# Kernel optimization log

Hardware: AMD Instinct MI355X
Metric: run time of the kernel (lower is better)

## Reference

```python
import jax, jax.numpy as jnp
import numpy as np

jax.config.update("jax_enable_x64", True)  # FixedPointMul math is done in float64, as in torch

B, S, H = 8, 4096, 768


def setup_inputs():
    key = jax.random.key(0)
    k = jax.random.split(key, 6)
    s_act = jnp.array([4.0 / 127.0], dtype=jnp.float32)  # per-tensor 8-bit activation scale

    def qact(kk):  # produce int8-quantized-looking activations
        x = jax.random.normal(kk, (B, S, H), jnp.float32)
        return s_act * jnp.clip(jnp.round(x / s_act), -128, 127)

    return {
        "hidden_states": qact(k[0]),
        "hidden_states_scaling_factor": s_act,
        "input_tensor": qact(k[1]),
        "input_tensor_scaling_factor": s_act,
        "dense_weight": 0.02 * jax.random.normal(k[2], (H, H), jnp.float32),
        "dense_bias": 0.01 * jax.random.normal(k[3], (H,), jnp.float32),
        "ln_weight": 1.0 + 0.05 * jax.random.normal(k[4], (H,), jnp.float32),
        "ln_bias": 0.05 * jax.random.normal(k[5], (H,), jnp.float32),
    }


def _sym_scale(k, smin, smax):
    n = 2 ** (k - 1) - 1
    return jnp.clip(jnp.maximum(jnp.abs(smin), jnp.abs(smax)), 1e-8, None) / n


def _sym_quant(x, k, scale):
    n = 2 ** (k - 1) - 1
    return jnp.clip(jnp.round(x / scale), -n, n - 1)


def _batch_frexp(x):
    # returns (round(mantissa * 2^31), 31 - exponent) as in ibert batch_frexp
    m, e = jnp.frexp(x)
    return jnp.floor(m * (2.0 ** 31) + 0.5), 31.0 - e


def _fixedpoint_mul(x, pre_scale, bit, z_scale, identity=None, id_scale=None):
    n = 2 ** (bit - 1) - 1
    ps = jnp.reshape(pre_scale, (1, 1, -1)).astype(jnp.float64)
    z = z_scale.astype(jnp.float64)
    z_int = jnp.round(x.astype(jnp.float64) / ps)
    m, e = _batch_frexp(ps / z)
    out = jnp.round(z_int * m / (2.0 ** e))
    if identity is not None:
        isf = jnp.reshape(id_scale, (1, 1, -1)).astype(jnp.float64)
        wx = jnp.round(identity.astype(jnp.float64) / isf)
        m1, e1 = _batch_frexp(isf / z)
        out = out + jnp.round(wx * m1 / (2.0 ** e1))
    return jnp.clip(out, -n - 1, n).astype(jnp.float32)


def _quant_act(x, bit, pre_scale, identity=None, id_scale=None):
    x_act = x if identity is None else x + identity
    s = _sym_scale(bit, x_act.min(), x_act.max())  # per-tensor scale (dynamic range)
    q = _fixedpoint_mul(x, pre_scale, bit, s, identity, id_scale)
    return q * s, s


def reference(hidden_states, hidden_states_scaling_factor, input_tensor, input_tensor_scaling_factor, dense_weight, dense_bias, ln_weight, ln_bias):
    # ---- QuantLinear: per-channel int8 weights, int32 bias ----
    w_min = dense_weight.min(axis=1)
    w_max = dense_weight.max(axis=1)
    fc_scale = _sym_scale(8, w_min, w_max)                      # [H_out]
    w_int = _sym_quant(dense_weight, 8, fc_scale[:, None])      # [H_out, H_in]
    bias_scale = fc_scale * hidden_states_scaling_factor        # [H_out]
    b_int = _sym_quant(dense_bias, 32, bias_scale)
    x_int = hidden_states / hidden_states_scaling_factor
    hs = (jnp.einsum("bsh,oh->bso", x_int, w_int) + b_int) * bias_scale
    # dropout: eval mode -> identity
    # ---- QuantAct(22-bit) with quantized residual add ----
    hs, ln_in_scale = _quant_act(hs, 22, bias_scale, input_tensor, input_tensor_scaling_factor)
    # ---- IntLayerNorm (integer-only LayerNorm) ----
    x_int = hs / ln_in_scale
    mean_int = jnp.round(jnp.mean(x_int, axis=2, keepdims=True))
    y_int = x_int - mean_int
    var0 = jnp.sum(y_int ** 2, axis=2, keepdims=True)
    shift = jnp.ceil(jnp.log2(jnp.sqrt(jnp.maximum(var0, 1.0) / 2.0 ** 32)))  # set_shift (max_bit=32)
    shift = jnp.maximum(0.0, shift.max())
    y_sh = jnp.floor(y_int / 2.0 ** shift)
    var_int = jnp.sum(y_sh ** 2, axis=2, keepdims=True)
    std_int = jnp.floor(jnp.sqrt(var_int)) * 2.0 ** shift
    factor = jnp.floor(2.0 ** 31 / std_int)
    y_int = jnp.floor(y_int * factor / 2.0)
    sf = jnp.sqrt(jnp.float32(H)) / 2.0 ** 30
    bias_int = jnp.floor((ln_bias / ln_weight) / sf)
    y_int = y_int + bias_int
    sf_out = sf * ln_weight                                     # [H]
    hs = y_int * sf_out
    # ---- QuantAct(8-bit) output requantization ----
    hs, out_scale = _quant_act(hs, 8, sf_out)
    return hs, out_scale
```

## Files before the change

### kernel.cpp

```cpp
#include <hip/hip_runtime.h>

typedef int   v4i   __attribute__((ext_vector_type(4)));
typedef unsigned long u64x2 __attribute__((ext_vector_type(2)));

#define HDIM 768
#define NTOK 32768

static constexpr size_t WX_OFF   = 0;
static constexpr size_t WINT_OFF = 25165824;
static constexpr size_t FACT_OFF = WINT_OFF + 589824;
static constexpr size_t RS1_OFF  = WINT_OFF + 1179648;
static constexpr size_t RS2_OFF  = RS1_OFF + 6144;
static constexpr size_t BS_OFF   = RS2_OFF + 6144;
static constexpr size_t BINT_OFF = BS_OFF + 3072;
static constexpr size_t LNBI_OFF = BINT_OFF + 3072;
static constexpr size_t SFO_OFF  = LNBI_OFF + 3072;
static constexpr size_t SC_OFF   = SFO_OFF + 3072;
static constexpr size_t RSM1_OFF = SC_OFF + 64;

__device__ __forceinline__ unsigned fenc(float f) {
    unsigned u = __float_as_uint(f);
    return (u >> 31) ? ~u : (u | 0x80000000u);
}
__device__ __forceinline__ float fdec(unsigned e) {
    unsigned u = (e >> 31) ? (e & 0x7fffffffu) : ~e;
    return __uint_as_float(u);
}

#define GLDS16(g, l) __builtin_amdgcn_global_load_lds( \
    (const __attribute__((address_space(1))) unsigned int*)(g), \
    (__attribute__((address_space(3))) unsigned int*)(l), 16, 0, 0)

__device__ __forceinline__ int swz4(int r) { return (r & 3) ^ ((r >> 2) & 3); }

__global__ __launch_bounds__(256) void k0_prep(const float* __restrict__ W,
                                               const float* __restrict__ bias,
                                               const float* __restrict__ ln_w,
                                               const float* __restrict__ ln_b,
                                               const float* __restrict__ phsf,
                                               char* __restrict__ ws) {
    int o = blockIdx.x, tid = threadIdx.x;
    __shared__ float red[256];
    __shared__ float fc_sh;
    float m = 0.f;
    for (int j = tid; j < HDIM; j += 256) m = fmaxf(m, fabsf(W[(size_t)o * HDIM + j]));
    red[tid] = m;
    __syncthreads();
    for (int s = 128; s; s >>= 1) { if (tid < s) red[tid] = fmaxf(red[tid], red[tid + s]); __syncthreads(); }
    if (tid == 0) {
        float fc = fmaxf(red[0], 1e-8f) / 127.0f;
        float hsf = *phsf;
        float bs = fc * hsf;
        fc_sh = fc;
        ((float*)(ws + BS_OFF))[o] = bs;
        ((int*)(ws + BINT_OFF))[o] = (int)rintf(bias[o] / bs);
        float sf = sqrtf(768.0f) / 1073741824.0f;
        float lw = ln_w[o], lb = ln_b[o];
        ((int*)(ws + LNBI_OFF))[o] = (int)floorf((lb / lw) / sf);
        ((float*)(ws + SFO_OFF))[o] = sf * lw;
    }
    __syncthreads();
    float fc = fc_sh;
    char* w8 = (char*)(ws + WINT_OFF);
    for (int j = tid; j < HDIM; j += 256) {
        float q = rintf(W[(size_t)o * HDIM + j] / fc);
        q = fminf(fmaxf(q, -127.f), 126.f);
        w8[(size_t)o * HDIM + j] = (char)q;
    }
    if (blockIdx.x == 0 && tid < 8) {
        unsigned* sc = (unsigned*)(ws + SC_OFF);
        unsigned v = 0u;
        if (tid == 0 || tid == 2) v = 0xFFFFFFFFu;
        sc[tid] = v;
    }
}

__global__ __launch_bounds__(256) void kp_a8(const float* __restrict__ hs,
                                             const float* __restrict__ phsf,
                                             char* __restrict__ ws) {
    int idx = blockIdx.x * 256 + threadIdx.x;
    float inv = 1.0f / *phsf;
    const float4* in4 = (const float4*)hs + (size_t)idx * 4;
    unsigned ow[4];
    #pragma unroll
    for (int j = 0; j < 4; ++j) {
        float4 v = in4[j];
        int q0 = (int)rintf(v.x * inv), q1 = (int)rintf(v.y * inv);
        int q2 = (int)rintf(v.z * inv), q3 = (int)rintf(v.w * inv);
        ow[j] = (unsigned)(q0 & 255) | ((unsigned)(q1 & 255) << 8) |
                ((unsigned)(q2 & 255) << 16) | ((unsigned)(q3 & 255) << 24);
    }
    ((uint4*)(ws + WX_OFF))[idx] = make_uint4(ow[0], ow[1], ow[2], ow[3]);
}

#define BM 128
#define BN 192
#define BK 64
#define NKT (HDIM / BK)
__global__ __launch_bounds__(256) void k1_gemm(const float* __restrict__ inp,
                                               char* __restrict__ ws,
                                               int* __restrict__ accOut) {
    __shared__ alignas(16) char As[2][BM * BK];
    __shared__ alignas(16) char Bs[2][BN * BK];
    __shared__ float rmn[4], rmx[4];
    int tid = threadIdx.x, lane = tid & 63, wave = tid >> 6;
    int wrow = lane & 15, g = lane >> 4;
    int bid = blockIdx.x;
    int xcd = bid & 7, slot = bid >> 3;
    int mtile = xcd * 32 + (slot >> 2);
    int ntile = slot & 3;
    int t0 = mtile * BM, o0 = ntile * BN;
    const char* a8 = (const char*)(ws + WX_OFF);
    const char* w8 = (const char*)(ws + WINT_OFF);

    const char* asrc[2]; const char* bsrc[3];
    int aldso[2], bldso[3];
    #pragma unroll
    for (int i = 0; i < 2; ++i) {
        int c = i * 256 + tid, r = c >> 2, s = c & 3;
        asrc[i] = a8 + (size_t)(t0 + r) * HDIM + (s ^ swz4(r)) * 16;
        aldso[i] = (i * 256 + wave * 64) * 16;
    }
    #pragma unroll
    for (int i = 0; i < 3; ++i) {
        int c = i * 256 + tid, r = c >> 2, s = c & 3;
        bsrc[i] = w8 + (size_t)(o0 + r) * HDIM + (s ^ swz4(r)) * 16;
        bldso[i] = (i * 256 + wave * 64) * 16;
    }

    int wm = wave & 1, wn = wave >> 1;
    int aofs[4], bofs[6];
    #pragma unroll
    for (int mi = 0; mi < 4; ++mi) { int r = wm * 64 + mi * 16 + wrow; aofs[mi] = r * BK + ((g ^ swz4(r)) * 16); }
    #pragma unroll
    for (int nf = 0; nf < 6; ++nf) { int r = wn * 96 + nf * 16 + wrow; bofs[nf] = r * BK + ((g ^ swz4(r)) * 16); }

    #pragma unroll
    for (int i = 0; i < 2; ++i) GLDS16(asrc[i], &As[0][aldso[i]]);
    #pragma unroll
    for (int i = 0; i < 3; ++i) GLDS16(bsrc[i], &Bs[0][bldso[i]]);
    #pragma unroll
    for (int i = 0; i < 2; ++i) GLDS16(asrc[i] + BK, &As[1][aldso[i]]);
    #pragma unroll
    for (int i = 0; i < 3; ++i) GLDS16(bsrc[i] + BK, &Bs[1][bldso[i]]);
    asm volatile("s_waitcnt vmcnt(5)" ::: "memory");
    __builtin_amdgcn_s_barrier();

    v4i acc[4][6] = {};
    for (int kt = 0; kt < NKT; ++kt) {
        int cur = kt & 1;
        u64x2 af[4], bf[6];
        #pragma unroll
        for (int mi = 0; mi < 4; ++mi) af[mi] = *(const u64x2*)&As[cur][aofs[mi]];
        #pragma unroll
        for (int nf = 0; nf < 6; ++nf) bf[nf] = *(const u64x2*)&Bs[cur][bofs[nf]];
        asm volatile("s_waitcnt lgkmcnt(0)" ::: "memory");
        __builtin_amdgcn_s_barrier();
        if (kt + 2 < NKT) {
            #pragma unroll
            for (int i = 0; i < 2; ++i) GLDS16(asrc[i] + (kt + 2) * BK, &As[cur][aldso[i]]);
            #pragma unroll
            for (int i = 0; i < 3; ++i) GLDS16(bsrc[i] + (kt + 2) * BK, &Bs[cur][bldso[i]]);
        }
        __builtin_amdgcn_s_setprio(1);
        #pragma unroll
        for (int mi = 0; mi < 4; ++mi)
            #pragma unroll
            for (int nf = 0; nf < 6; ++nf) {
                acc[mi][nf] = __builtin_amdgcn_mfma_i32_16x16x32_i8((long)af[mi][0], (long)bf[nf][0], acc[mi][nf], 0, 0, 0);
                acc[mi][nf] = __builtin_amdgcn_mfma_i32_16x16x32_i8((long)af[mi][1], (long)bf[nf][1], acc[mi][nf], 0, 0, 0);
            }
        __builtin_amdgcn_s_setprio(0);
        if (kt + 2 < NKT) {
            asm volatile("s_waitcnt vmcnt(5)" ::: "memory");
            __builtin_amdgcn_s_barrier();
        } else if (kt + 2 == NKT) {
            asm volatile("s_waitcnt vmcnt(0)" ::: "memory");
            __builtin_amdgcn_s_barrier();
        }
    }

    const float* bscale = (const float*)(ws + BS_OFF);
    const int* bint = (const int*)(ws + BINT_OFF);
    int oo[6]; float bsc[6]; int bi[6];
    #pragma unroll
    for (int nf = 0; nf < 6; ++nf) {
        oo[nf] = o0 + wn * 96 + nf * 16 + wrow;
        bsc[nf] = bscale[oo[nf]];
        bi[nf]  = bint[oo[nf]];
    }
    float lmn = 3.402823466e38f, lmx = -3.402823466e38f;
    #pragma unroll
    for (int mi = 0; mi < 4; ++mi)
        #pragma unroll
        for (int r = 0; r < 4; ++r) {
            int t = t0 + wm * 64 + mi * 16 + g * 4 + r;
            size_t rb = (size_t)t * HDIM;
            #pragma unroll
            for (int nf = 0; nf < 6; ++nf) {
                int a = acc[mi][nf][r] + bi[nf];
                size_t idx = rb + oo[nf];
                accOut[idx] = a;
                float xa = (float)a * bsc[nf] + inp[idx];
                lmn = fminf(lmn, xa);
                lmx = fmaxf(lmx, xa);
            }
        }
    #pragma unroll
    for (int off = 32; off; off >>= 1) {
        lmn = fminf(lmn, __shfl_down(lmn, off));
        lmx = fmaxf(lmx, __shfl_down(lmx, off));
    }
    if (lane == 0) { rmn[wave] = lmn; rmx[wave] = lmx; }
    __syncthreads();
    if (tid == 0) {
        float mn = fminf(fminf(rmn[0], rmn[1]), fminf(rmn[2], rmn[3]));
        float mx = fmaxf(fmaxf(rmx[0], rmx[1]), fmaxf(rmx[2], rmx[3]));
        volatile unsigned* sc = (volatile unsigned*)(ws + SC_OFF);
        unsigned emn = fenc(mn), emx = fenc(mx);
        if (emn < sc[0]) atomicMin((unsigned*)&sc[0], emn);
        if (emx > sc[1]) atomicMax((unsigned*)&sc[1], emx);
    }
}

__global__ __launch_bounds__(256) void k2_scale1(const float* __restrict__ pisf, char* __restrict__ ws) {
    __shared__ float s_sh;
    unsigned* sc = (unsigned*)(ws + SC_OFF);
    if (threadIdx.x == 0) {
        float mn = fdec(sc[0]), mx = fdec(sc[1]);
        float s = fmaxf(fmaxf(fabsf(mn), fabsf(mx)), 1e-8f) / 2097151.0f;
        ((float*)sc)[5] = s;
        s_sh = s;
        double r = (double)(*pisf) / (double)s;
        int ex; double mant = frexp(r, &ex);
        double m1 = floor(mant * 2147483648.0 + 0.5);
        ((double*)(ws + RSM1_OFF))[0] = m1 * exp2((double)(ex - 31));
    }
    __syncthreads();
    float s = s_sh;
    const float* bs = (const float*)(ws + BS_OFF);
    double* rs1 = (double*)(ws + RS1_OFF);
    for (int o = threadIdx.x; o < HDIM; o += 256) {
        double r = (double)bs[o] / (double)s;
        int ex; double mant = frexp(r, &ex);
        double m = floor(mant * 2147483648.0 + 0.5);
        rs1[o] = m * exp2((double)(ex - 31));
    }
}

__global__ __launch_bounds__(256) void k3_rows(char* __restrict__ ws, int* __restrict__ buf,
                                               const float* __restrict__ inp,
                                               const float* __restrict__ pisf) {
    int tid = threadIdx.x, lane = tid & 63, wave = tid >> 6;
    int wid = blockIdx.x * 4 + wave;
    const double* rs1 = (const double*)(ws + RS1_OFF);
    double rsm1 = *(const double*)(ws + RSM1_OFF);
    float inv_isf = 1.0f / *pisf;
    double t_rs1[12];
    #pragma unroll
    for (int c = 0; c < 3; ++c) {
        int o0 = (lane + 64 * c) * 4;
        #pragma unroll
        for (int j = 0; j < 4; ++j) t_rs1[c * 4 + j] = rs1[o0 + j];
    }
    int localShift = 0;
    int4 aP[3]; float4 xP[3];
    {
        size_t b0 = (size_t)(wid * 4) * HDIM;
        #pragma unroll
        for (int c = 0; c < 3; ++c) {
            aP[c] = ((const int4*)(buf + b0))[lane + 64 * c];
            xP[c] = ((const float4*)(inp + b0))[lane + 64 * c];
        }
    }
    for (int rr = 0; rr < 4; ++rr) {
        int4 aN[3]; float4 xN[3];
        if (rr < 3) {
            size_t nb = (size_t)(wid * 4 + rr + 1) * HDIM;
            #pragma unroll
            for (int c = 0; c < 3; ++c) {
                aN[c] = ((const int4*)(buf + nb))[lane + 64 * c];
                xN[c] = ((const float4*)(inp + nb))[lane + 64 * c];
            }
        }
        size_t base = (size_t)(wid * 4 + rr) * HDIM;
        int q[12];
        int sum = 0;
        #pragma unroll
        for (int c = 0; c < 3; ++c) {
            int av[4] = {aP[c].x, aP[c].y, aP[c].z, aP[c].w};
            float xv[4] = {xP[c].x, xP[c].y, xP[c].z, xP[c].w};
            #pragma unroll
            for (int j = 0; j < 4; ++j) {
                double q1 = rint((double)av[j] * t_rs1[c * 4 + j]);
                int wxj = (int)rintf(xv[j] * inv_isf);
                double qq = q1 + rint((double)wxj * rsm1);
                qq = fmin(fmax(qq, -2097152.0), 2097151.0);
                q[c * 4 + j] = (int)qq;
                sum += q[c * 4 + j];
            }
        }
        #pragma unroll
        for (int off = 32; off; off >>= 1) sum += __shfl_xor(sum, off);
        int mean = (int)rint((double)sum / 768.0);
        long long var0 = 0;
        #pragma unroll
        for (int k = 0; k < 12; ++k) { q[k] -= mean; var0 += (long long)q[k] * (long long)q[k]; }
        #pragma unroll
        for (int off = 32; off; off >>= 1) var0 += __shfl_xor(var0, off);
        #pragma unroll
        for (int c = 0; c < 3; ++c) {
            int4 y = {q[c * 4 + 0], q[c * 4 + 1], q[c * 4 + 2], q[c * 4 + 3]};
            ((int4*)(buf + base))[lane + 64 * c] = y;
        }
        if (lane == 0) {
            double v = (double)(var0 < 1 ? 1LL : var0);
            int sr = (int)ceil(0.5 * log2(v) - 16.0);
            localShift = max(localShift, sr);
        }
        #pragma unroll
        for (int c = 0; c < 3; ++c) { aP[c] = aN[c]; xP[c] = xN[c]; }
    }
    if (lane == 0 && localShift > 0) {
        int* sp = (int*)(ws + SC_OFF) + 4;
        if (localShift > *(volatile int*)sp) atomicMax(sp, localShift);
    }
}

__global__ __launch_bounds__(256) void k4_rows(char* __restrict__ ws, const int* __restrict__ buf) {
    int tid = threadIdx.x, lane = tid & 63, wave = tid >> 6;
    int wid = blockIdx.x * 4 + wave;
    int shift = *(((const int*)(ws + SC_OFF)) + 4);
    const int* lnbi = (const int*)(ws + LNBI_OFF);
    const float* sfo = (const float*)(ws + SFO_OFF);
    __shared__ float rmn[4], rmx[4];
    int t_lnbi[12]; float t_sfo[12];
    #pragma unroll
    for (int c = 0; c < 3; ++c) {
        int o0 = (lane + 64 * c) * 4;
        #pragma unroll
        for (int j = 0; j < 4; ++j) { t_lnbi[c * 4 + j] = lnbi[o0 + j]; t_sfo[c * 4 + j] = sfo[o0 + j]; }
    }
    unsigned* fact = (unsigned*)(ws + FACT_OFF);
    float lmn = 3.402823466e38f, lmx = -3.402823466e38f;
    int4 yP[3];
    {
        size_t b0 = (size_t)(wid * 4) * HDIM;
        #pragma unroll
        for (int c = 0; c < 3; ++c) yP[c] = ((const int4*)(buf + b0))[lane + 64 * c];
    }
    for (int rr = 0; rr < 4; ++rr) {
        int4 yN[3];
        if (rr < 3) {
            size_t nb = (size_t)(wid * 4 + rr + 1) * HDIM;
            #pragma unroll
            for (int c = 0; c < 3; ++c) yN[c] = ((const int4*)(buf + nb))[lane + 64 * c];
        }
        int yv[12];
        #pragma unroll
        for (int c = 0; c < 3; ++c) {
            yv[c * 4 + 0] = yP[c].x; yv[c * 4 + 1] = yP[c].y; yv[c * 4 + 2] = yP[c].z; yv[c * 4 + 3] = yP[c].w;
        }
        long long var = 0;
        #pragma unroll
        for (int k = 0; k < 12; ++k) { int ysh = yv[k] >> shift; var += (long long)ysh * (long long)ysh; }
        #pragma unroll
        for (int off = 32; off; off >>= 1) var += __shfl_xor(var, off);
        double std_int = floor(sqrt((double)var)) * (double)(1LL << shift);
        if (std_int < 1.0) std_int = 1.0;
        long long factor = (long long)floor(2147483648.0 / std_int);
        if (lane == 0) fact[wid * 4 + rr] = (unsigned)factor;
        #pragma unroll
        for (int k = 0; k < 12; ++k) {
            long long t = ((long long)yv[k] * factor) >> 1;
            int v2 = (int)t + t_lnbi[k];
            float h = (float)v2 * t_sfo[k];
            lmn = fminf(lmn, h);
            lmx = fmaxf(lmx, h);
        }
        #pragma unroll
        for (int c = 0; c < 3; ++c) yP[c] = yN[c];
    }
    #pragma unroll
    for (int off = 32; off; off >>= 1) {
        lmn = fminf(lmn, __shfl_xor(lmn, off));
        lmx = fmaxf(lmx, __shfl_xor(lmx, off));
    }
    if (lane == 0) { rmn[wave] = lmn; rmx[wave] = lmx; }
    __syncthreads();
    if (tid == 0) {
        float mn = fminf(fminf(rmn[0], rmn[1]), fminf(rmn[2], rmn[3]));
        float mx = fmaxf(fmaxf(rmx[0], rmx[1]), fmaxf(rmx[2], rmx[3]));
        volatile unsigned* sc = (volatile unsigned*)(ws + SC_OFF);
        unsigned emn = fenc(mn), emx = fenc(mx);
        if (emn < sc[2]) atomicMin((unsigned*)&sc[2], emn);
        if (emx > sc[3]) atomicMax((unsigned*)&sc[3], emx);
    }
}

__global__ __launch_bounds__(256) void k5_scale2(char* __restrict__ ws) {
    __shared__ float s_sh;
    unsigned* sc = (unsigned*)(ws + SC_OFF);
    if (threadIdx.x == 0) {
        float mn = fdec(sc[2]), mx = fdec(sc[3]);
        float s2 = fmaxf(fmaxf(fabsf(mn), fabsf(mx)), 1e-8f) / 127.0f;
        ((float*)sc)[6] = s2;
        s_sh = s2;
    }
    __syncthreads();
    float s2 = s_sh;
    const float* sfo = (const float*)(ws + SFO_OFF);
    double* rs2 = (double*)(ws + RS2_OFF);
    for (int o = threadIdx.x; o < HDIM; o += 256) {
        double r = (double)sfo[o] / (double)s2;
        int ex; double mant = frexp(r, &ex);
        double m = floor(mant * 2147483648.0 + 0.5);
        rs2[o] = m * exp2((double)(ex - 31));
    }
}

__global__ __launch_bounds__(256) void k6_out(char* __restrict__ ws, float* __restrict__ out) {
    int tid = threadIdx.x, lane = tid & 63, wave = tid >> 6;
    int wid = blockIdx.x * 4 + wave;
    const double* rs2 = (const double*)(ws + RS2_OFF);
    const int* lnbi = (const int*)(ws + LNBI_OFF);
    const unsigned* fact = (const unsigned*)(ws + FACT_OFF);
    float s2 = ((const float*)(ws + SC_OFF))[6];
    double t_rs2[12]; int t_lnbi[12];
    #pragma unroll
    for (int c = 0; c < 3; ++c) {
        int o0 = (lane + 64 * c) * 4;
        #pragma unroll
        for (int j = 0; j < 4; ++j) { t_rs2[c * 4 + j] = rs2[o0 + j]; t_lnbi[c * 4 + j] = lnbi[o0 + j]; }
    }
    int* buf = (int*)out;
    int4 yP[3];
    {
        size_t b0 = (size_t)(wid * 4) * HDIM;
        #pragma unroll
        for (int c = 0; c < 3; ++c) yP[c] = ((const int4*)(buf + b0))[lane + 64 * c];
    }
    for (int rr = 0; rr < 4; ++rr) {
        int4 yN[3];
        if (rr < 3) {
            size_t nb = (size_t)(wid * 4 + rr + 1) * HDIM;
            #pragma unroll
            for (int c = 0; c < 3; ++c) yN[c] = ((const int4*)(buf + nb))[lane + 64 * c];
        }
        size_t base = (size_t)(wid * 4 + rr) * HDIM;
        long long factor = (long long)fact[wid * 4 + rr];
        int yv[12];
        #pragma unroll
        for (int c = 0; c < 3; ++c) {
            yv[c * 4 + 0] = yP[c].x; yv[c * 4 + 1] = yP[c].y; yv[c * 4 + 2] = yP[c].z; yv[c * 4 + 3] = yP[c].w;
        }
        #pragma unroll
        for (int c = 0; c < 3; ++c) {
            float4 r;
            float* rp = &r.x;
            #pragma unroll
            for (int j = 0; j < 4; ++j) {
                int k = c * 4 + j;
                long long t = ((long long)yv[k] * factor) >> 1;
                int v2 = (int)t + t_lnbi[k];
                double q = rint((double)v2 * t_rs2[k]);
                q = fmin(fmax(q, -128.0), 127.0);
                rp[j] = (float)q * s2;
            }
            ((float4*)(out + base))[lane + 64 * c] = r;
        }
        #pragma unroll
        for (int c = 0; c < 3; ++c) yP[c] = yN[c];
    }
    if (wid == 0 && tid == 0) out[(size_t)NTOK * HDIM] = s2;
}

extern "C" void kernel_launch(void* const* d_in, const int* in_sizes, int n_in,
                              void* d_out, int out_size, void* d_ws, size_t ws_size,
                              hipStream_t stream) {
    const float* hs   = (const float*)d_in[0];
    const float* phsf = (const float*)d_in[1];
    const float* inp  = (const float*)d_in[2];
    const float* pisf = (const float*)d_in[3];
    const float* W    = (const float*)d_in[4];
    const float* bias = (const float*)d_in[5];
    const float* ln_w = (const float*)d_in[6];
    const float* ln_b = (const float*)d_in[7];
    char* ws = (char*)d_ws;
    float* out = (float*)d_out;
    int* buf = (int*)d_out;

    k0_prep<<<HDIM, 256, 0, stream>>>(W, bias, ln_w, ln_b, phsf, ws);
    kp_a8<<<NTOK * HDIM / 4096, 256, 0, stream>>>(hs, phsf, ws);
    k1_gemm<<<(NTOK / BM) * (HDIM / BN), 256, 0, stream>>>(inp, ws, buf);
    k2_scale1<<<1, 256, 0, stream>>>(pisf, ws);
    k3_rows<<<NTOK / 16, 256, 0, stream>>>(ws, buf, inp, pisf);
    k4_rows<<<NTOK / 16, 256, 0, stream>>>(ws, buf);
    k5_scale2<<<1, 256, 0, stream>>>(ws);
    k6_out<<<NTOK / 16, 256, 0, stream>>>(ws, out);
}
```

Measured before the change: 412.7 us.

## Quantize residual input to int8 once and stage GEMM epilogue through LDS

The activation prep kernel now also quantizes the residual input to int8 in workspace. The GEMM epilogue and the first row kernel then read 1 byte per element instead of a float. The GEMM epilogue writes accumulators into shared memory and re-reads them as row-contiguous int4 chunks, which gives coalesced global stores and loads. The int8 path is gated on workspace size, which adds an extra buffer and extra barriers in the epilogue.

```diff
diff --git a/kernel.cpp b/kernel.cpp
--- a/kernel.cpp
+++ b/kernel.cpp
@@ -17,6 +17,8 @@
 static constexpr size_t SFO_OFF  = LNBI_OFF + 3072;
 static constexpr size_t SC_OFF   = SFO_OFF + 3072;
 static constexpr size_t RSM1_OFF = SC_OFF + 64;
+static constexpr size_t INP8_OFF = RSM1_OFF + 64;
+static constexpr size_t WS_NEED8 = INP8_OFF + (size_t)NTOK * HDIM;
 
 __device__ __forceinline__ unsigned fenc(float f) {
     unsigned u = __float_as_uint(f);
@@ -75,34 +77,57 @@
     }
 }
 
+template<int U8>
 __global__ __launch_bounds__(256) void kp_a8(const float* __restrict__ hs,
+                                             const float* __restrict__ inp,
                                              const float* __restrict__ phsf,
+                                             const float* __restrict__ pisf,
                                              char* __restrict__ ws) {
     int idx = blockIdx.x * 256 + threadIdx.x;
-    float inv = 1.0f / *phsf;
-    const float4* in4 = (const float4*)hs + (size_t)idx * 4;
+    float invh = 1.0f / *phsf;
+    const float4* h4 = (const float4*)hs + (size_t)idx * 4;
     unsigned ow[4];
     #pragma unroll
     for (int j = 0; j < 4; ++j) {
-        float4 v = in4[j];
-        int q0 = (int)rintf(v.x * inv), q1 = (int)rintf(v.y * inv);
-        int q2 = (int)rintf(v.z * inv), q3 = (int)rintf(v.w * inv);
+        float4 v = h4[j];
+        int q0 = (int)rintf(v.x * invh), q1 = (int)rintf(v.y * invh);
+        int q2 = (int)rintf(v.z * invh), q3 = (int)rintf(v.w * invh);
         ow[j] = (unsigned)(q0 & 255) | ((unsigned)(q1 & 255) << 8) |
                 ((unsigned)(q2 & 255) << 16) | ((unsigned)(q3 & 255) << 24);
     }
     ((uint4*)(ws + WX_OFF))[idx] = make_uint4(ow[0], ow[1], ow[2], ow[3]);
+    if (U8) {
+        float invi = 1.0f / *pisf;
+        const float4* x4 = (const float4*)inp + (size_t)idx * 4;
+        unsigned oi[4];
+        #pragma unroll
+        for (int j = 0; j < 4; ++j) {
+            float4 v = x4[j];
+            int q0 = (int)rintf(v.x * invi), q1 = (int)rintf(v.y * invi);
+            int q2 = (int)rintf(v.z * invi), q3 = (int)rintf(v.w * invi);
+            oi[j] = (unsigned)(q0 & 255) | ((unsigned)(q1 & 255) << 8) |
+                    ((unsigned)(q2 & 255) << 16) | ((unsigned)(q3 & 255) << 24);
+        }
+        ((uint4*)(ws + INP8_OFF))[idx] = make_uint4(oi[0], oi[1], oi[2], oi[3]);
+    }
 }
 
 #define BM 128
 #define BN 192
 #define BK 64
 #define NKT (HDIM / BK)
+#define SROW 196
+template<int U8>
 __global__ __launch_bounds__(256) void k1_gemm(const float* __restrict__ inp,
+                                               const char* __restrict__ i8,
+                                               const float* __restrict__ pisf,
                                                char* __restrict__ ws,
                                                int* __restrict__ accOut) {
-    __shared__ alignas(16) char As[2][BM * BK];
-    __shared__ alignas(16) char Bs[2][BN * BK];
-    __shared__ float rmn[4], rmx[4];
+    __shared__ alignas(16) char smem[40992];
+    char* As0 = smem;
+    char* Bs0 = smem + 16384;
+    float* rmn = (float*)(smem + 40960);
+    float* rmx = rmn + 4;
     int tid = threadIdx.x, lane = tid & 63, wave = tid >> 6;
     int wrow = lane & 15, g = lane >> 4;
     int bid = blockIdx.x;
@@ -136,31 +161,33 @@
     for (int nf = 0; nf < 6; ++nf) { int r = wn * 96 + nf * 16 + wrow; bofs[nf] = r * BK + ((g ^ swz4(r)) * 16); }
 
     #pragma unroll
-    for (int i = 0; i < 2; ++i) GLDS16(asrc[i], &As[0][aldso[i]]);
-    #pragma unroll
-    for (int i = 0; i < 3; ++i) GLDS16(bsrc[i], &Bs[0][bldso[i]]);
-    #pragma unroll
-    for (int i = 0; i < 2; ++i) GLDS16(asrc[i] + BK, &As[1][aldso[i]]);
-    #pragma unroll
-    for (int i = 0; i < 3; ++i) GLDS16(bsrc[i] + BK, &Bs[1][bldso[i]]);
+    for (int i = 0; i < 2; ++i) GLDS16(asrc[i], As0 + aldso[i]);
+    #pragma unroll
+    for (int i = 0; i < 3; ++i) GLDS16(bsrc[i], Bs0 + bldso[i]);
+    #pragma unroll
+    for (int i = 0; i < 2; ++i) GLDS16(asrc[i] + BK, As0 + 8192 + aldso[i]);
+    #pragma unroll
+    for (int i = 0; i < 3; ++i) GLDS16(bsrc[i] + BK, Bs0 + 12288 + bldso[i]);
     asm volatile("s_waitcnt vmcnt(5)" ::: "memory");
     __builtin_amdgcn_s_barrier();
 
     v4i acc[4][6] = {};
     for (int kt = 0; kt < NKT; ++kt) {
         int cur = kt & 1;
+        const char* Ac = As0 + cur * 8192;
+        const char* Bc = Bs0 + cur * 12288;
         u64x2 af[4], bf[6];
         #pragma unroll
-        for (int mi = 0; mi < 4; ++mi) af[mi] = *(const u64x2*)&As[cur][aofs[mi]];
-        #pragma unroll
-        for (int nf = 0; nf < 6; ++nf) bf[nf] = *(const u64x2*)&Bs[cur][bofs[nf]];
+        for (int mi = 0; mi < 4; ++mi) af[mi] = *(const u64x2*)(Ac + aofs[mi]);
+        #pragma unroll
+        for (int nf = 0; nf < 6; ++nf) bf[nf] = *(const u64x2*)(Bc + bofs[nf]);
         asm volatile("s_waitcnt lgkmcnt(0)" ::: "memory");
         __builtin_amdgcn_s_barrier();
         if (kt + 2 < NKT) {
             #pragma unroll
-            for (int i = 0; i < 2; ++i) GLDS16(asrc[i] + (kt + 2) * BK, &As[cur][aldso[i]]);
-            #pragma unroll
-            for (int i = 0; i < 3; ++i) GLDS16(bsrc[i] + (kt + 2) * BK, &Bs[cur][bldso[i]]);
+            for (int i = 0; i < 2; ++i) GLDS16(asrc[i] + (kt + 2) * BK, As0 + cur * 8192 + aldso[i]);
+            #pragma unroll
+            for (int i = 0; i < 3; ++i) GLDS16(bsrc[i] + (kt + 2) * BK, Bs0 + cur * 12288 + bldso[i]);
         }
         __builtin_amdgcn_s_setprio(1);
         #pragma unroll
@@ -182,35 +209,54 @@
 
     const float* bscale = (const float*)(ws + BS_OFF);
     const int* bint = (const int*)(ws + BINT_OFF);
-    int oo[6]; float bsc[6]; int bi[6];
-    #pragma unroll
-    for (int nf = 0; nf < 6; ++nf) {
-        oo[nf] = o0 + wn * 96 + nf * 16 + wrow;
-        bsc[nf] = bscale[oo[nf]];
-        bi[nf]  = bint[oo[nf]];
-    }
+    float isf = U8 ? *pisf : 0.f;
+    int* sAcc = (int*)smem;
     float lmn = 3.402823466e38f, lmx = -3.402823466e38f;
     #pragma unroll
-    for (int mi = 0; mi < 4; ++mi)
-        #pragma unroll
-        for (int r = 0; r < 4; ++r) {
-            int t = t0 + wm * 64 + mi * 16 + g * 4 + r;
-            size_t rb = (size_t)t * HDIM;
-            #pragma unroll
-            for (int nf = 0; nf < 6; ++nf) {
-                int a = acc[mi][nf][r] + bi[nf];
-                size_t idx = rb + oo[nf];
-                accOut[idx] = a;
-                float xa = (float)a * bsc[nf] + inp[idx];
-                lmn = fminf(lmn, xa);
-                lmx = fmaxf(lmx, xa);
+    for (int mi = 0; mi < 4; ++mi) {
+        __syncthreads();
+        #pragma unroll
+        for (int nf = 0; nf < 6; ++nf)
+            #pragma unroll
+            for (int r = 0; r < 4; ++r)
+                sAcc[(wm * 16 + g * 4 + r) * SROW + wn * 96 + nf * 16 + wrow] = acc[mi][nf][r];
+        __syncthreads();
+        #pragma unroll
+        for (int k = 0; k < 6; ++k) {
+            int i4 = tid + k * 256;
+            int sr = i4 / 48, c4 = i4 - sr * 48;
+            int t = t0 + (sr >> 4) * 64 + mi * 16 + (sr & 15);
+            int col = o0 + c4 * 4;
+            int4 a4 = *(const int4*)&sAcc[sr * SROW + c4 * 4];
+            int4 b4 = *(const int4*)&bint[col];
+            float4 bs4 = *(const float4*)&bscale[col];
+            a4.x += b4.x; a4.y += b4.y; a4.z += b4.z; a4.w += b4.w;
+            size_t idx = (size_t)t * HDIM + col;
+            *(int4*)&accOut[idx] = a4;
+            float x0, x1, x2, x3;
+            if (U8) {
+                unsigned w = *(const unsigned*)(i8 + idx);
+                x0 = (float)(int)(char)(w) * isf;
+                x1 = (float)(int)(char)(w >> 8) * isf;
+                x2 = (float)(int)(char)(w >> 16) * isf;
+                x3 = (float)(int)(char)(w >> 24) * isf;
+            } else {
+                float4 x4 = *(const float4*)&inp[idx];
+                x0 = x4.x; x1 = x4.y; x2 = x4.z; x3 = x4.w;
             }
-        }
+            float xa;
+            xa = (float)a4.x * bs4.x + x0; lmn = fminf(lmn, xa); lmx = fmaxf(lmx, xa);
+            xa = (float)a4.y * bs4.y + x1; lmn = fminf(lmn, xa); lmx = fmaxf(lmx, xa);
+            xa = (float)a4.z * bs4.z + x2; lmn = fminf(lmn, xa); lmx = fmaxf(lmx, xa);
+            xa = (float)a4.w * bs4.w + x3; lmn = fminf(lmn, xa); lmx = fmaxf(lmx, xa);
+        }
+    }
     #pragma unroll
     for (int off = 32; off; off >>= 1) {
         lmn = fminf(lmn, __shfl_down(lmn, off));
         lmx = fmaxf(lmx, __shfl_down(lmx, off));
     }
+    __syncthreads();
     if (lane == 0) { rmn[wave] = lmn; rmx[wave] = lmx; }
     __syncthreads();
     if (tid == 0) {
@@ -248,8 +294,10 @@
     }
 }
 
+template<int U8>
 __global__ __launch_bounds__(256) void k3_rows(char* __restrict__ ws, int* __restrict__ buf,
                                                const float* __restrict__ inp,
+                                               const char* __restrict__ i8,
                                                const float* __restrict__ pisf) {
     int tid = threadIdx.x, lane = tid & 63, wave = tid >> 6;
     int wid = blockIdx.x * 4 + wave;
@@ -264,23 +312,25 @@
         for (int j = 0; j < 4; ++j) t_rs1[c * 4 + j] = rs1[o0 + j];
     }
     int localShift = 0;
-    int4 aP[3]; float4 xP[3];
+    int4 aP[3]; float4 xP[3]; int wP[3];
     {
         size_t b0 = (size_t)(wid * 4) * HDIM;
         #pragma unroll
         for (int c = 0; c < 3; ++c) {
             aP[c] = ((const int4*)(buf + b0))[lane + 64 * c];
-            xP[c] = ((const float4*)(inp + b0))[lane + 64 * c];
+            if (U8) wP[c] = ((const int*)(i8 + b0))[lane + 64 * c];
+            else    xP[c] = ((const float4*)(inp + b0))[lane + 64 * c];
         }
     }
     for (int rr = 0; rr < 4; ++rr) {
-        int4 aN[3]; float4 xN[3];
+        int4 aN[3]; float4 xN[3]; int wN[3];
         if (rr < 3) {
             size_t nb = (size_t)(wid * 4 + rr + 1) * HDIM;
             #pragma unroll
             for (int c = 0; c < 3; ++c) {
                 aN[c] = ((const int4*)(buf + nb))[lane + 64 * c];
-                xN[c] = ((const float4*)(inp + nb))[lane + 64 * c];
+                if (U8) wN[c] = ((const int*)(i8 + nb))[lane + 64 * c];
+                else    xN[c] = ((const float4*)(inp + nb))[lane + 64 * c];
             }
         }
         size_t base = (size_t)(wid * 4 + rr) * HDIM;
@@ -289,11 +339,15 @@
         #pragma unroll
         for (int c = 0; c < 3; ++c) {
             int av[4] = {aP[c].x, aP[c].y, aP[c].z, aP[c].w};
-            float xv[4] = {xP[c].x, xP[c].y, xP[c].z, xP[c].w};
             #pragma unroll
             for (int j = 0; j < 4; ++j) {
                 double q1 = rint((double)av[j] * t_rs1[c * 4 + j]);
-                int wxj = (int)rintf(xv[j] * inv_isf);
+                int wxj;
+                if (U8) wxj = (int)(char)(wP[c] >> (8 * j));
+                else {
+                    float xv = (j == 0) ? xP[c].x : (j == 1) ? xP[c].y : (j == 2) ? xP[c].z : xP[c].w;
+                    wxj = (int)rintf(xv * inv_isf);
+                }
                 double qq = q1 + rint((double)wxj * rsm1);
                 qq = fmin(fmax(qq, -2097152.0), 2097151.0);
                 q[c * 4 + j] = (int)qq;
@@ -319,7 +373,7 @@
             localShift = max(localShift, sr);
         }
         #pragma unroll
-        for (int c = 0; c < 3; ++c) { aP[c] = aN[c]; xP[c] = xN[c]; }
+        for (int c = 0; c < 3; ++c) { aP[c] = aN[c]; xP[c] = xN[c]; wP[c] = wN[c]; }
     }
     if (lane == 0 && localShift > 0) {
         int* sp = (int*)(ws + SC_OFF) + 4;
@@ -392,9 +446,10 @@
         float mn = fminf(fminf(rmn[0], rmn[1]), fminf(rmn[2], rmn[3]));
         float mx = fmaxf(fmaxf(rmx[0], rmx[1]), fmaxf(rmx[2], rmx[3]));
         volatile unsigned* sc = (volatile unsigned*)(ws + SC_OFF);
-        unsigned emn = fenc(mn), emx = fenc(mx);
+        unsigned emn = fenc(lmn), emx2 = fenc(lmx);
+        emn = fenc(mn); emx2 = fenc(mx);
         if (emn < sc[2]) atomicMin((unsigned*)&sc[2], emn);
-        if (emx > sc[3]) atomicMax((unsigned*)&sc[3], emx);
+        if (emx2 > sc[3]) atomicMax((unsigned*)&sc[3], emx2);
     }
 }
 
@@ -489,12 +544,21 @@
     char* ws = (char*)d_ws;
     float* out = (float*)d_out;
     int* buf = (int*)d_out;
+    const char* i8 = (const char*)(ws + INP8_OFF);
+    bool use8 = ws_size >= WS_NEED8;
 
     k0_prep<<<HDIM, 256, 0, stream>>>(W, bias, ln_w, ln_b, phsf, ws);
-    kp_a8<<<NTOK * HDIM / 4096, 256, 0, stream>>>(hs, phsf, ws);
-    k1_gemm<<<(NTOK / BM) * (HDIM / BN), 256, 0, stream>>>(inp, ws, buf);
-    k2_scale1<<<1, 256, 0, stream>>>(pisf, ws);
-    k3_rows<<<NTOK / 16, 256, 0, stream>>>(ws, buf, inp, pisf);
+    if (use8) {
+        kp_a8<1><<<NTOK * HDIM / 4096, 256, 0, stream>>>(hs, inp, phsf, pisf, ws);
+        k1_gemm<1><<<(NTOK / BM) * (HDIM / BN), 256, 0, stream>>>(inp, i8, pisf, ws, buf);
+        k2_scale1<<<1, 256, 0, stream>>>(pisf, ws);
+        k3_rows<1><<<NTOK / 16, 256, 0, stream>>>(ws, buf, inp, i8, pisf);
+    } else {
+        kp_a8<0><<<NTOK * HDIM / 4096, 256, 0, stream>>>(hs, inp, phsf, pisf, ws);
+        k1_gemm<0><<<(NTOK / BM) * (HDIM / BN), 256, 0, stream>>>(inp, i8, pisf, ws, buf);
+        k2_scale1<<<1, 256, 0, stream>>>(pisf, ws);
+        k3_rows<0><<<NTOK / 16, 256, 0, stream>>>(ws, buf, inp, i8, pisf);
+    }
     k4_rows<<<NTOK / 16, 256, 0, stream>>>(ws, buf);
     k5_scale2<<<1, 256, 0, stream>>>(ws);
     k6_out<<<NTOK / 16, 256, 0, stream>>>(ws, out);
```

New measurement: 443.5 us. 1.07x slower.
